# Optimization experiments

Measured on AMD Instinct MI355X. Metric: run time of the kernel, lower is better.

The kernel has to match this reference:

```python
import jax, jax.numpy as jnp
import numpy as np

PQ_M = 8
VALS_PER_DIM = 256
SUB_DIM = 64
EMB = PQ_M * SUB_DIM  # 512
NUM_ITEMS = 1_000_000
BATCH = 256
SEQ = 512


def setup_inputs() -> dict:
    key = jax.random.key(0)
    k1, k2, k3 = jax.random.split(key, 3)
    input_ids = jax.random.randint(k1, (BATCH, SEQ), 0, NUM_ITEMS, dtype=jnp.int64 if jax.config.jax_enable_x64 else jnp.int32).astype(jnp.int32)
    item_codes = jax.random.randint(k2, (NUM_ITEMS, PQ_M), 0, VALS_PER_DIM, dtype=jnp.int32)
    centroids = jax.random.normal(k3, (PQ_M, VALS_PER_DIM, SUB_DIM), dtype=jnp.float32)
    # module zeroes centroid index 0 in every subspace at init
    centroids = centroids.at[:, 0, :].set(0.0)
    return {"input_ids": input_ids, "item_codes": item_codes, "centroids": centroids}


def reference(input_ids, item_codes, centroids):
    # input_ids: [B, S] int; item_codes: [N, M] int32; centroids: [M, V, D] f32
    codes = item_codes[input_ids]                       # [B, S, M]
    codes = jnp.minimum(codes, VALS_PER_DIM - 1)        # clamp per subspace
    byte_idx = jnp.arange(PQ_M, dtype=jnp.int32)        # [M]
    # per-subspace gather: centroids[m, codes[b,s,m]] -> [B, S, M, D]
    sub = centroids[byte_idx[None, None, :], codes]
    B, S = input_ids.shape
    result = sub.reshape(B, S, EMB)                     # concat subspaces
    pad = (input_ids == 0)[:, :, None]                  # zero padding tokens
    return jnp.where(pad, 0.0, result)
```

## Files before the change

kernel.cpp:

```cpp
#include <hip/hip_runtime.h>


#define VALS_ 256
#define NTOK_ (256 * 512)
#define TOKS_BLK 64
#define TOK_CHUNK 16
#define CHUNKS (TOKS_BLK / TOK_CHUNK)
#define THREADS 256
#define ITERS (TOK_CHUNK * 128 / THREADS)

typedef float f4 __attribute__((ext_vector_type(4)));

__global__ __launch_bounds__(THREADS) void ItemCode_kernel(
    const int* __restrict__ input_ids,
    const int* __restrict__ item_codes,
    const float* __restrict__ centroids,
    float* __restrict__ out)
{
    __shared__ int s_cidx[2][TOK_CHUNK * 8];

    const int tid = threadIdx.x;
    const int blk_tok0 = blockIdx.x * TOKS_BLK;

    const int pt = tid >> 3;
    const int pm = tid & 7;
    const bool stager = (tid < TOK_CHUNK * 8);

    const int e  = tid & 127;
    const int m  = e >> 4;
    const int s4 = e & 15;
    const int t0 = tid >> 7;

    const f4* __restrict__ cent4 = reinterpret_cast<const f4*>(centroids);
    f4* __restrict__ out4 = reinterpret_cast<f4*>(out);

    auto gather = [&](int c) -> int {
        const int id = input_ids[blk_tok0 + c * TOK_CHUNK + pt];
        int code = __builtin_nontemporal_load(&item_codes[id * 8 + pm]);
        code = min(code, VALS_ - 1);
        code = (id == 0) ? 0 : code;
        return ((pm << 8) + code) << 4;
    };

    int reg;
    if (stager) {
        reg = gather(0);
        s_cidx[0][tid] = reg;
    }

    for (int c = 0; c < CHUNKS; ++c) {
        __syncthreads();
        const bool more = (c + 1 < CHUNKS);
        if (more && stager) reg = gather(c + 1);

        const int buf = c & 1;
        const int ob = (blk_tok0 + c * TOK_CHUNK) * 128;
        #pragma unroll
        for (int it = 0; it < ITERS; ++it) {
            const int t  = t0 + it * 2;
            const int ci = s_cidx[buf][(t << 3) | m] + s4;
            __builtin_nontemporal_store(cent4[ci], &out4[ob + tid + it * THREADS]);
        }
        if (more && stager) s_cidx[buf ^ 1][tid] = reg;
    }
}

extern "C" void kernel_launch(void* const* d_in, const int* in_sizes, int n_in,
                              void* d_out, int out_size, void* d_ws, size_t ws_size,
                              hipStream_t stream) {
    const int*   input_ids  = (const int*)d_in[0];
    const int*   item_codes = (const int*)d_in[1];
    const float* centroids  = (const float*)d_in[2];
    float*       out        = (float*)d_out;

    dim3 grid(NTOK_ / TOKS_BLK), block(THREADS);
    ItemCode_kernel<<<grid, block, 0, stream>>>(input_ids, item_codes, centroids, out);
}
```

Measured before the change: 63.65 us.

## Replace chunked double-buffered staging with single-shot 32-token blocks

Removes the 4-chunk double-buffered pipeline that overlapped code gathering with output writes. Each block now handles 32 tokens: every thread gathers one code, there is one barrier, and then a fully unrolled copy of 16 iterations. Output stores become regular stores instead of nontemporal. This doubles the grid size and cuts barriers per block, but gives up the in-block overlap of gather latency and changes how the output writes are cached.

```diff
diff --git a/kernel.cpp b/kernel.cpp
--- a/kernel.cpp
+++ b/kernel.cpp
@@ -3,11 +3,9 @@
 
 #define VALS_ 256
 #define NTOK_ (256 * 512)
-#define TOKS_BLK 64
-#define TOK_CHUNK 16
-#define CHUNKS (TOKS_BLK / TOK_CHUNK)
+#define TOKS_BLK 32
 #define THREADS 256
-#define ITERS (TOK_CHUNK * 128 / THREADS)
+#define ITERS (TOKS_BLK * 128 / THREADS)
 
 typedef float f4 __attribute__((ext_vector_type(4)));
 
@@ -17,51 +15,36 @@
     const float* __restrict__ centroids,
     float* __restrict__ out)
 {
-    __shared__ int s_cidx[2][TOK_CHUNK * 8];
+    __shared__ int s_off[TOKS_BLK * 8];
 
     const int tid = threadIdx.x;
-    const int blk_tok0 = blockIdx.x * TOKS_BLK;
+    const int tok0 = blockIdx.x * TOKS_BLK;
 
-    const int pt = tid >> 3;
-    const int pm = tid & 7;
-    const bool stager = (tid < TOK_CHUNK * 8);
+    {
+        const int pt = tid >> 3;
+        const int pm = tid & 7;
+        const int id = input_ids[tok0 + pt];
+        int code = __builtin_nontemporal_load(&item_codes[id * 8 + pm]);
+        code = min(code, VALS_ - 1);
+        code = id ? code : 0;
+        s_off[tid] = ((pm << 8) + code) << 4;
+    }
+    __syncthreads();
 
     const int e  = tid & 127;
     const int m  = e >> 4;
+    const int t0 = tid >> 7;
     const int s4 = e & 15;
-    const int t0 = tid >> 7;
 
     const f4* __restrict__ cent4 = reinterpret_cast<const f4*>(centroids);
     f4* __restrict__ out4 = reinterpret_cast<f4*>(out);
+    const int ob = tok0 * 128;
 
-    auto gather = [&](int c) -> int {
-        const int id = input_ids[blk_tok0 + c * TOK_CHUNK + pt];
-        int code = __builtin_nontemporal_load(&item_codes[id * 8 + pm]);
-        code = min(code, VALS_ - 1);
-        code = (id == 0) ? 0 : code;
-        return ((pm << 8) + code) << 4;
-    };
-
-    int reg;
-    if (stager) {
-        reg = gather(0);
-        s_cidx[0][tid] = reg;
-    }
-
-    for (int c = 0; c < CHUNKS; ++c) {
-        __syncthreads();
-        const bool more = (c + 1 < CHUNKS);
-        if (more && stager) reg = gather(c + 1);
-
-        const int buf = c & 1;
-        const int ob = (blk_tok0 + c * TOK_CHUNK) * 128;
-        #pragma unroll
-        for (int it = 0; it < ITERS; ++it) {
-            const int t  = t0 + it * 2;
-            const int ci = s_cidx[buf][(t << 3) | m] + s4;
-            __builtin_nontemporal_store(cent4[ci], &out4[ob + tid + it * THREADS]);
-        }
-        if (more && stager) s_cidx[buf ^ 1][tid] = reg;
+    #pragma unroll
+    for (int it = 0; it < ITERS; ++it) {
+        const int t  = t0 + it * 2;
+        const int ci = s_off[(t << 3) | m] + s4;
+        out4[ob + tid + it * THREADS] = cent4[ci];
     }
 }
 
```

New measurement: 59.73 us. 6.2% less time.
